# Kernel optimization log

Measured on AMD Instinct MI355X. Metric: run time of the kernel, lower is better.

## Reference

```python
import jax, jax.numpy as jnp
import numpy as np

K = 64            # number of keypoints
PATCH = 16        # patch size
NUM_CLASSES = 1000
K_HARRIS = 0.04


def _conv3x3(x, w):
    # x: [N, Cin, H, W], w: [Cout, Cin, 3, 3], stride 1, padding 1 (torch conv2d = cross-correlation)
    return jax.lax.conv_general_dilated(x, w, (1, 1), 'SAME',
                                        dimension_numbers=('NCHW', 'OIHW', 'NCHW'))


def _harris_coords(x, k, patch_size):
    B, C, H, W = x.shape
    g = jnp.mean(x, axis=1, keepdims=True) if C != 1 else x  # grayscale [B,1,H,W]
    dxk = jnp.array([[-1., 0., 1.], [-1., 0., 1.], [-1., 0., 1.]], x.dtype).reshape(1, 1, 3, 3)
    dyk = jnp.array([[-1., -1., -1.], [0., 0., 0.], [1., 1., 1.]], x.dtype).reshape(1, 1, 3, 3)
    gauss = (jnp.array([[1., 2., 1.], [2., 4., 2.], [1., 2., 1.]], x.dtype) / 16.0).reshape(1, 1, 3, 3)
    dx = _conv3x3(g, dxk)
    dy = _conv3x3(g, dyk)
    Sxx = _conv3x3(dx * dx, gauss)
    Syy = _conv3x3(dy * dy, gauss)
    Sxy = _conv3x3(dx * dy, gauss)
    R = Sxx * Syy - Sxy ** 2 - K_HARRIS * (Sxx + Syy) ** 2  # [B,1,H,W]
    m = patch_size
    mask = jnp.zeros((H, W), x.dtype).at[m:H - m, m:W - m].set(1.0)
    R_flat = (R[:, 0] * mask).reshape(B, -1)
    _, idx = jax.lax.top_k(R_flat, k)                        # [B,k]
    coords = jnp.stack([idx // W, idx % W], axis=-1).astype(jnp.float32)  # (row, col)
    coords = (coords / jnp.array([H, W], jnp.float32) - 0.5) * 2.0
    return jnp.clip(coords, -1.0, 1.0)                       # [B,k,2]


def _grid_sample_bilinear(img, grid):
    # img: [N,C,H,W]; grid: [N,Hg,Wg,2] with (x, y) in [-1,1]; align_corners=True, zeros padding
    N, C, H, W = img.shape
    Hg, Wg = grid.shape[1], grid.shape[2]
    gx = (grid[..., 0] + 1.0) * 0.5 * (W - 1)
    gy = (grid[..., 1] + 1.0) * 0.5 * (H - 1)
    x0 = jnp.floor(gx); y0 = jnp.floor(gy)
    x1 = x0 + 1.0;      y1 = y0 + 1.0
    wx1 = gx - x0; wx0 = 1.0 - wx1
    wy1 = gy - y0; wy0 = 1.0 - wy1

    img_flat = img.reshape(N, C, H * W)

    def gather(xi, yi):
        valid = ((xi >= 0) & (xi < W) & (yi >= 0) & (yi < H)).astype(img.dtype)
        xc = jnp.clip(xi, 0, W - 1).astype(jnp.int32)
        yc = jnp.clip(yi, 0, H - 1).astype(jnp.int32)
        flat = (yc * W + xc).reshape(N, 1, Hg * Wg)
        vals = jnp.take_along_axis(img_flat, flat, axis=2).reshape(N, C, Hg, Wg)
        return vals * valid[:, None]

    out = (gather(x0, y0) * (wx0 * wy0)[:, None]
           + gather(x1, y0) * (wx1 * wy0)[:, None]
           + gather(x0, y1) * (wx0 * wy1)[:, None]
           + gather(x1, y1) * (wx1 * wy1)[:, None])
    return out


def _extract_patches(images, keypoints, patch_size):
    B, C, H, W = images.shape
    k = keypoints.shape[1]
    coords01 = (keypoints + 1.0) / 2.0                       # [B,k,2] (y,x) in [0,1]
    r = patch_size / H
    pg = jnp.linspace(-r, r, patch_size)
    yy, xx = jnp.meshgrid(pg, pg, indexing='ij')
    base = jnp.stack([xx, yy], axis=-1)[None, None]          # [1,1,P,P,2] (x_off, y_off)
    grid = base + coords01[:, :, None, None, :]              # faithful to original broadcast
    grid = grid * 2.0 - 1.0
    grid = grid.reshape(B * k, patch_size, patch_size, 2)
    x_exp = jnp.repeat(images, k, axis=0)                    # repeat_interleave on batch
    patches = _grid_sample_bilinear(x_exp, grid)             # [B*k,C,P,P]
    return patches.reshape(B, k, C, patch_size, patch_size)


def _classify(patches, conv_w, conv_b, fc1_w, fc1_b, fc2_w, fc2_b):
    B, k, C, H, W = patches.shape
    p = patches.reshape(B * k, C, H, W)
    h = _conv3x3(p, conv_w) + conv_b[None, :, None, None]
    h = jax.nn.relu(h)
    h = h.reshape(B * k, -1)                                 # [B*k, 8*P*P]
    h = jax.nn.relu(h @ fc1_w.T + fc1_b)                     # [B*k, 64]
    h = h.reshape(B, k * 64)
    return h @ fc2_w.T + fc2_b                               # [B, num_classes]


def setup_inputs() -> dict:
    key = jax.random.key(0)
    ks = jax.random.split(key, 7)
    B, C, H, W = 32, 3, 224, 224
    return {
        'x': jax.random.normal(ks[0], (B, C, H, W), dtype=jnp.float32),
        'conv_w': jax.random.normal(ks[1], (8, C, 3, 3), dtype=jnp.float32) * 0.1,
        'conv_b': jax.random.normal(ks[2], (8,), dtype=jnp.float32) * 0.05,
        'fc1_w': jax.random.normal(ks[3], (64, 8 * PATCH * PATCH), dtype=jnp.float32) * 0.02,
        'fc1_b': jax.random.normal(ks[4], (64,), dtype=jnp.float32) * 0.05,
        'fc2_w': jax.random.normal(ks[5], (NUM_CLASSES, 64 * K), dtype=jnp.float32) * 0.02,
        'fc2_b': jax.random.normal(ks[6], (NUM_CLASSES,), dtype=jnp.float32) * 0.05,
    }


def reference(x, conv_w, conv_b, fc1_w, fc1_b, fc2_w, fc2_b):
    coords = _harris_coords(x, K, PATCH)                     # [B,K,2]
    patches = _extract_patches(x, coords, PATCH)             # [B,K,C,P,P]
    return _classify(patches, conv_w, conv_b, fc1_w, fc1_b, fc2_w, fc2_b)
```

## Files before the change

kernel.cpp:

```cpp
#include <hip/hip_runtime.h>
#include <cstdint>
#include <math.h>

#define HW 224
#define NPIX (HW*HW)
#define BATCH 32
#define KP 64
#define PS 16
#define NCLS 1000
#define TKB 56
#define FC1_KS 16

__device__ __forceinline__ uint64_t tk_pack(float v, int idx) {
    uint32_t u = __float_as_uint(v);
    u = (u & 0x80000000u) ? ~u : (u | 0x80000000u);
    return ((uint64_t)u << 32) | (uint32_t)(~idx);
}

template<int S>
__device__ __forceinline__ uint64_t sx64(uint64_t k) {
    uint32_t lo = (uint32_t)k, hi = (uint32_t)(k >> 32);
    if constexpr (S == 1) {
        lo = (uint32_t)__builtin_amdgcn_mov_dpp((int)lo, 0xB1, 0xF, 0xF, true);
        hi = (uint32_t)__builtin_amdgcn_mov_dpp((int)hi, 0xB1, 0xF, 0xF, true);
    } else if constexpr (S == 2) {
        lo = (uint32_t)__builtin_amdgcn_mov_dpp((int)lo, 0x4E, 0xF, 0xF, true);
        hi = (uint32_t)__builtin_amdgcn_mov_dpp((int)hi, 0x4E, 0xF, 0xF, true);
    } else if constexpr (S <= 16) {
        constexpr int imm = (S << 10) | 0x1F;
        lo = (uint32_t)__builtin_amdgcn_ds_swizzle((int)lo, imm);
        hi = (uint32_t)__builtin_amdgcn_ds_swizzle((int)hi, imm);
    } else {
        lo = (uint32_t)__shfl_xor((int)lo, 32, 64);
        hi = (uint32_t)__shfl_xor((int)hi, 32, 64);
    }
    return ((uint64_t)hi << 32) | lo;
}

#define BSTAGE(SIZE, S) { uint64_t o = sx64<S>(k); \
    bool keepmax = (((lane & S) != 0) == ((lane & SIZE) == 0)); \
    k = keepmax ? (k > o ? k : o) : (k < o ? k : o); }

__device__ __forceinline__ uint64_t tk_sort_asc(uint64_t k, int lane) {
    BSTAGE(2,1)
    BSTAGE(4,2)  BSTAGE(4,1)
    BSTAGE(8,4)  BSTAGE(8,2)  BSTAGE(8,1)
    BSTAGE(16,8) BSTAGE(16,4) BSTAGE(16,2) BSTAGE(16,1)
    BSTAGE(32,16) BSTAGE(32,8) BSTAGE(32,4) BSTAGE(32,2) BSTAGE(32,1)
    BSTAGE(64,32) BSTAGE(64,16) BSTAGE(64,8) BSTAGE(64,4) BSTAGE(64,2) BSTAGE(64,1)
    return k;
}

#define CSTAGE(S) { uint64_t o = sx64<S>(k); \
    bool keepmax = ((lane & S) == 0); \
    k = keepmax ? (k > o ? k : o) : (k < o ? k : o); }

__device__ __forceinline__ uint64_t tk_clean_desc(uint64_t k, int lane) {
    CSTAGE(32) CSTAGE(16) CSTAGE(8) CSTAGE(4) CSTAGE(2) CSTAGE(1)
    return k;
}

__global__ __launch_bounds__(256) void k_harris_topk(const float* __restrict__ x,
                                                     uint64_t* __restrict__ cand) {
    const int r = blockIdx.x, b = blockIdx.y;
    const int tid = threadIdx.x;
    const int row0 = r * 4;
    __shared__ float G[8][228];
    __shared__ float DXs[6][228];
    __shared__ float DYs[6][228];
    __shared__ float RB[896];
    __shared__ uint64_t SM[4][64];
    const float* xb = x + (size_t)b * 3 * NPIX;

    for (int l = tid; l < 8 * 224; l += 256) {
        int gr = l / 224, gc = l % 224;
        int gy = row0 - 2 + gr;
        float v = 0.f;
        if (gy >= 0 && gy < HW) {
            int o = gy * HW + gc;
            v = (xb[o] + xb[NPIX + o] + xb[2 * NPIX + o]) / 3.0f;
        }
        G[gr][gc + 1] = v;
    }
    if (tid < 8) { G[tid][0] = 0.f; G[tid][225] = 0.f; }
    if (tid < 6) { DXs[tid][0] = 0.f; DXs[tid][225] = 0.f;
                   DYs[tid][0] = 0.f; DYs[tid][225] = 0.f; }
    __syncthreads();

    if (tid < 192) {
        int dr = tid >> 5, cb = (tid & 31) * 7;
        int ay = row0 - 1 + dr;
        float g0[9], g1[9], g2[9];
        #pragma unroll
        for (int v = 0; v < 9; v++) {
            g0[v] = G[dr][cb + v];
            g1[v] = G[dr + 1][cb + v];
            g2[v] = G[dr + 2][cb + v];
        }
        bool ok = (ay >= 0 && ay < HW);
        #pragma unroll
        for (int t = 0; t < 7; t++) {
            float dxv = 0.f, dyv = 0.f;
            if (ok) {
                dxv = (g0[t + 2] - g0[t]) + (g1[t + 2] - g1[t]) +
                      (g2[t + 2] - g2[t]);
                dyv = (g2[t] + g2[t + 1] + g2[t + 2]) -
                      (g0[t] + g0[t + 1] + g0[t + 2]);
            }
            DXs[dr][cb + t + 1] = dxv;
            DYs[dr][cb + t + 1] = dyv;
        }
    }
    __syncthreads();

    if (tid < 128) {
        const int rr = tid >> 5, cb = (tid & 31) * 7;
        const int gy = row0 + rr;
        float dxw[3][9], dyw[3][9];
        #pragma unroll
        for (int u = 0; u < 3; u++)
            #pragma unroll
            for (int v = 0; v < 9; v++) {
                dxw[u][v] = DXs[rr + u][cb + v];
                dyw[u][v] = DYs[rr + u][cb + v];
            }
        const bool rowok = (gy >= PS && gy < HW - PS);
        const float gw[3][3] = {{1.f/16.f, 2.f/16.f, 1.f/16.f},
                                {2.f/16.f, 4.f/16.f, 2.f/16.f},
                                {1.f/16.f, 2.f/16.f, 1.f/16.f}};
        #pragma unroll
        for (int t = 0; t < 7; t++) {
            int c = cb + t;
            float outv = 0.f;
            if (rowok && c >= PS && c < HW - PS) {
                float sxx = 0.f, syy = 0.f, sxy = 0.f;
                #pragma unroll
                for (int u = 0; u < 3; u++)
                    #pragma unroll
                    for (int v = 0; v < 3; v++) {
                        float dv = dxw[u][t + v];
                        float ev = dyw[u][t + v];
                        float w = gw[u][v];
                        sxx += w * dv * dv;
                        syy += w * ev * ev;
                        sxy += w * dv * ev;
                    }
                float tr = sxx + syy;
                outv = sxx * syy - sxy * sxy - 0.04f * tr * tr;
            }
            RB[rr * 224 + c] = outv;
        }
    }
    __syncthreads();

    const int w = tid >> 6, lane = tid & 63;
    const int gbase = (row0 + w) * 224;
    uint64_t T = 0;
    #pragma unroll 1
    for (int it = 0; it < 4; it++) {
        int px = it * 64 + lane;
        uint64_t ck = 0;
        if (px < 224) ck = tk_pack(RB[w * 224 + px], gbase + px);
        uint64_t thr = __shfl(T, 63, 64);
        if (__ballot(ck > thr)) {
            uint64_t s = tk_sort_asc(ck, lane);
            uint64_t m = (T > s) ? T : s;
            T = tk_clean_desc(m, lane);
        }
    }

    SM[w][lane] = T;
    __syncthreads();
    if (w == 0 || w == 2) {
        uint64_t C = SM[w + 1][63 - lane];
        uint64_t m = (T > C) ? T : C;
        T = tk_clean_desc(m, lane);
        SM[w][lane] = T;
    }
    __syncthreads();
    if (w == 0) {
        uint64_t C = SM[2][63 - lane];
        uint64_t m = (T > C) ? T : C;
        T = tk_clean_desc(m, lane);
        cand[((size_t)b * TKB + r) * 64 + lane] = T;
    }
}

__global__ __launch_bounds__(512) void k_topk_merge(const uint64_t* __restrict__ cand,
                                                    int* __restrict__ kp) {
    const int img = blockIdx.x;
    const int w = threadIdx.x >> 6, lane = threadIdx.x & 63;
    const uint64_t* cb = cand + (size_t)img * TKB * 64;
    __shared__ uint64_t S[8][64];

    uint64_t T = cb[(w * 7) * 64 + lane];
    #pragma unroll
    for (int r = 1; r < 7; r++) {
        uint64_t C = cb[(w * 7 + r) * 64 + (63 - lane)];
        uint64_t m = (T > C) ? T : C;
        T = tk_clean_desc(m, lane);
    }
    S[w][lane] = T;
    __syncthreads();
    if (w == 0) {
        #pragma unroll
        for (int r = 1; r < 8; r++) {
            uint64_t C = S[r][63 - lane];
            uint64_t m = (T > C) ? T : C;
            T = tk_clean_desc(m, lane);
        }
        kp[img * KP + lane] = (int)(~(uint32_t)T);
    }
}

__device__ __forceinline__ float gat4(const float* img, float xf, float yf) {
    bool valid = (xf >= 0.f) && (xf < 224.f) && (yf >= 0.f) && (yf < 224.f);
    if (!valid) return 0.f;
    int xi = (int)fminf(fmaxf(xf, 0.f), 223.f);
    int yi = (int)fminf(fmaxf(yf, 0.f), 223.f);
    return img[yi * HW + xi];
}

__global__ __launch_bounds__(256) void k_patch_conv(
    const float* __restrict__ x, const int* __restrict__ kp,
    const float* __restrict__ conv_w, const float* __restrict__ conv_b,
    float* __restrict__ h) {
    const int s = blockIdx.x;
    const int b = blockIdx.y;
    const int tid = threadIdx.x;

    __shared__ float P[3][18][18];

    const int idx = kp[b * KP + s];
    const int row = idx / HW, col = idx % HW;
    float cy = ((float)row / 224.0f - 0.5f) * 2.0f;
    float cx = ((float)col / 224.0f - 0.5f) * 2.0f;
    cy = fminf(fmaxf(cy, -1.0f), 1.0f);
    cx = fminf(fmaxf(cx, -1.0f), 1.0f);
    const float y01 = (cy + 1.0f) * 0.5f;
    const float x01 = (cx + 1.0f) * 0.5f;
    const float rr = 16.0f / 224.0f;
    const float step = (2.0f * rr) / 15.0f;
    const float* xb = x + (size_t)b * 3 * NPIX;

    for (int e = tid; e < 972; e += 256) {
        int c = e / 324, rem = e - c * 324;
        int yy = rem / 18, xx = rem - yy * 18;
        float val = 0.f;
        if (yy >= 1 && yy <= 16 && xx >= 1 && xx <= 16) {
            int i = yy - 1, j = xx - 1;
            float pj = (j == 15) ? rr : (-rr + (float)j * step);
            float pi = (i == 15) ? rr : (-rr + (float)i * step);
            float gxn = (pj + y01) * 2.0f - 1.0f;
            float gyn = (pi + x01) * 2.0f - 1.0f;
            float gx = (gxn + 1.0f) * 0.5f * 223.0f;
            float gy = (gyn + 1.0f) * 0.5f * 223.0f;
            float x0 = floorf(gx), y0 = floorf(gy);
            float x1 = x0 + 1.0f, y1 = y0 + 1.0f;
            float wx1 = gx - x0, wy1 = gy - y0;
            float wx0 = 1.0f - wx1, wy0 = 1.0f - wy1;
            const float* img = xb + (size_t)c * NPIX;
            val = gat4(img, x0, y0) * (wx0 * wy0)
                + gat4(img, x1, y0) * (wx1 * wy0)
                + gat4(img, x0, y1) * (wx0 * wy1)
                + gat4(img, x1, y1) * (wx1 * wy1);
        }
        P[c][yy][xx] = val;
    }
    __syncthreads();

    const int i = tid >> 4, j = tid & 15;
    float acc[8];
    #pragma unroll
    for (int co = 0; co < 8; co++) acc[co] = conv_b[co];
    #pragma unroll
    for (int ci = 0; ci < 3; ci++) {
        float n[9];
        #pragma unroll
        for (int di = 0; di < 3; di++)
            #pragma unroll
            for (int dj = 0; dj < 3; dj++)
                n[di * 3 + dj] = P[ci][i + di][j + dj];
        #pragma unroll
        for (int co = 0; co < 8; co++) {
            float a = acc[co];
            #pragma unroll
            for (int u = 0; u < 9; u++)
                a += n[u] * conv_w[co * 27 + ci * 9 + u];
            acc[co] = a;
        }
    }
    const size_t mbase = ((size_t)(b * KP + s)) * 2048;
    #pragma unroll
    for (int co = 0; co < 8; co++)
        h[mbase + co * 256 + tid] = fmaxf(acc[co], 0.0f);
}

__global__ __launch_bounds__(256) void k_fc1(
    const float* __restrict__ h, const float* __restrict__ fc1_w,
    float* __restrict__ partial) {
    const int mt = blockIdx.x;
    const int ks = blockIdx.y;
    const int tid = threadIdx.x;
    const int M0 = mt * 64;
    const int og = tid >> 4, mg = tid & 15;
    __shared__ float A[64 * 68];
    __shared__ float W[64 * 68];
    float acc[4][4];
    #pragma unroll
    for (int i = 0; i < 4; i++)
        #pragma unroll
        for (int j = 0; j < 4; j++) acc[i][j] = 0.f;

    #pragma unroll 1
    for (int ch = 0; ch < 2; ch++) {
        const int k0 = ks * 128 + ch * 64;
        __syncthreads();
        #pragma unroll
        for (int p = 0; p < 4; p++) {
            int row = p * 16 + (tid >> 4);
            int c0 = (tid & 15) * 4;
            float4 av = *(const float4*)&h[(size_t)(M0 + row) * 2048 + k0 + c0];
            A[(c0 + 0) * 68 + row] = av.x;
            A[(c0 + 1) * 68 + row] = av.y;
            A[(c0 + 2) * 68 + row] = av.z;
            A[(c0 + 3) * 68 + row] = av.w;
            float4 wv = *(const float4*)&fc1_w[(size_t)row * 2048 + k0 + c0];
            W[(c0 + 0) * 68 + row] = wv.x;
            W[(c0 + 1) * 68 + row] = wv.y;
            W[(c0 + 2) * 68 + row] = wv.z;
            W[(c0 + 3) * 68 + row] = wv.w;
        }
        __syncthreads();
        #pragma unroll 4
        for (int k = 0; k < 64; k++) {
            float4 a = *(float4*)&A[k * 68 + mg * 4];
            float4 w = *(float4*)&W[k * 68 + og * 4];
            acc[0][0] += a.x * w.x; acc[0][1] += a.x * w.y;
            acc[0][2] += a.x * w.z; acc[0][3] += a.x * w.w;
            acc[1][0] += a.y * w.x; acc[1][1] += a.y * w.y;
            acc[1][2] += a.y * w.z; acc[1][3] += a.y * w.w;
            acc[2][0] += a.z * w.x; acc[2][1] += a.z * w.y;
            acc[2][2] += a.z * w.z; acc[2][3] += a.z * w.w;
            acc[3][0] += a.w * w.x; acc[3][1] += a.w * w.y;
            acc[3][2] += a.w * w.z; acc[3][3] += a.w * w.w;
        }
    }
    float* pb = partial + ((size_t)ks * 2048 + M0) * 64;
    #pragma unroll
    for (int mi = 0; mi < 4; mi++) {
        float4 v = make_float4(acc[mi][0], acc[mi][1], acc[mi][2], acc[mi][3]);
        *(float4*)&pb[(mg * 4 + mi) * 64 + og * 4] = v;
    }
}

__global__ __launch_bounds__(256) void k_fc1_post(
    const float* __restrict__ partial, const float* __restrict__ fc1_b,
    const float* __restrict__ fc2_b, float* __restrict__ feat,
    float* __restrict__ out) {
    const int id = blockIdx.x * 256 + threadIdx.x;
    const int o = id & 63;
    float s = 0.f;
    #pragma unroll
    for (int ks = 0; ks < FC1_KS; ks++) s += partial[(size_t)ks * 131072 + id];
    s = fmaxf(s + fc1_b[o], 0.f);
    feat[id] = s;
    if (id < BATCH * NCLS) out[id] = fc2_b[id % NCLS];
}

__global__ __launch_bounds__(256) void k_fc2(
    const float* __restrict__ feat, const float* __restrict__ fc2_w,
    float* __restrict__ out) {
    const int c0 = blockIdx.x * 8;
    const int kbase = blockIdx.y * 256;
    const int tid = threadIdx.x;
    const int bq = tid & 7, kg = tid >> 3;

    __shared__ float U[8192];
    float* F2 = U;
    float* Wc = U + 32 * 132;
    float* Red = U;

    float4 acc[8];
    #pragma unroll
    for (int cl = 0; cl < 8; cl++) acc[cl] = make_float4(0.f, 0.f, 0.f, 0.f);

    #pragma unroll 1
    for (int ch = 0; ch < 2; ch++) {
        const int k0 = kbase + ch * 128;
        __syncthreads();
        #pragma unroll
        for (int it = 0; it < 4; it++) {
            int l = it * 256 + tid;
            int bb = l >> 5, kc = (l & 31) << 2;
            *(float4*)&F2[bb * 132 + kc] =
                *(const float4*)&feat[(size_t)bb * 4096 + k0 + kc];
        }
        {
            int cl = tid >> 5, kc = (tid & 31) << 2;
            *(float4*)&Wc[cl * 128 + kc] =
                *(const float4*)&fc2_w[(size_t)(c0 + cl) * 4096 + k0 + kc];
        }
        __syncthreads();
        float4 f0 = *(float4*)&F2[(bq * 4 + 0) * 132 + kg * 4];
        float4 f1 = *(float4*)&F2[(bq * 4 + 1) * 132 + kg * 4];
        float4 f2 = *(float4*)&F2[(bq * 4 + 2) * 132 + kg * 4];
        float4 f3 = *(float4*)&F2[(bq * 4 + 3) * 132 + kg * 4];
        #pragma unroll
        for (int cl = 0; cl < 8; cl++) {
            float4 w = *(float4*)&Wc[cl * 128 + kg * 4];
            acc[cl].x += w.x * f0.x + w.y * f0.y + w.z * f0.z + w.w * f0.w;
            acc[cl].y += w.x * f1.x + w.y * f1.y + w.z * f1.z + w.w * f1.w;
            acc[cl].z += w.x * f2.x + w.y * f2.y + w.z * f2.z + w.w * f2.w;
            acc[cl].w += w.x * f3.x + w.y * f3.y + w.z * f3.z + w.w * f3.w;
        }
    }

    __syncthreads();
    #pragma unroll
    for (int cl = 0; cl < 8; cl++)
        *(float4*)&Red[kg * 256 + cl * 32 + bq * 4] = acc[cl];
    __syncthreads();

    const int cl2 = tid >> 5, b2 = tid & 31;
    float s = 0.f;
    #pragma unroll
    for (int g = 0; g < 32; g++) s += Red[g * 256 + cl2 * 32 + b2];
    atomicAdd(&out[b2 * NCLS + c0 + cl2], s);
}

extern "C" void kernel_launch(void* const* d_in, const int* in_sizes, int n_in,
                              void* d_out, int out_size, void* d_ws, size_t ws_size,
                              hipStream_t stream) {
    const float* x      = (const float*)d_in[0];
    const float* conv_w = (const float*)d_in[1];
    const float* conv_b = (const float*)d_in[2];
    const float* fc1_w  = (const float*)d_in[3];
    const float* fc1_b  = (const float*)d_in[4];
    const float* fc2_w  = (const float*)d_in[5];
    const float* fc2_b  = (const float*)d_in[6];
    float* out = (float*)d_out;

    char* base = (char*)d_ws;
    const size_t region0 = (size_t)FC1_KS * 2048 * 64 * 4;
    uint64_t* cand    = (uint64_t*)base;
    float*    partial = (float*)base;
    float*    h       = (float*)(base + region0);
    float*    feat    = h + (size_t)2048 * 2048;
    int*      kp      = (int*)(feat + (size_t)4096 * 32);

    k_harris_topk<<<dim3(56, 32), 256, 0, stream>>>(x, cand);
    k_topk_merge<<<32, 512, 0, stream>>>(cand, kp);
    k_patch_conv<<<dim3(KP, BATCH), 256, 0, stream>>>(x, kp, conv_w, conv_b, h);
    k_fc1<<<dim3(32, FC1_KS), 256, 0, stream>>>(h, fc1_w, partial);
    k_fc1_post<<<512, 256, 0, stream>>>(partial, fc1_b, fc2_b, feat, out);
    k_fc2<<<dim3(125, 16), 256, 0, stream>>>(feat, fc2_w, out);
}
```

Baseline: 163.5 us.

## Retile Harris kernel into 8-row by 112-column blocks

```diff
diff --git a/kernel.cpp b/kernel.cpp
--- a/kernel.cpp
+++ b/kernel.cpp
@@ -62,67 +62,70 @@
 
 __global__ __launch_bounds__(256) void k_harris_topk(const float* __restrict__ x,
                                                      uint64_t* __restrict__ cand) {
-    const int r = blockIdx.x, b = blockIdx.y;
+    const int r = blockIdx.x;
+    const int hf = blockIdx.y;
+    const int b = blockIdx.z;
     const int tid = threadIdx.x;
-    const int row0 = r * 4;
-    __shared__ float G[8][228];
-    __shared__ float DXs[6][228];
-    __shared__ float DYs[6][228];
-    __shared__ float RB[896];
+    const int row0 = r * 8;
+    const int c0 = hf * 112;
+    __shared__ float U[12 * 120];
+    float (*G)[120] = (float(*)[120])U;
+    float* RB = U;
+    __shared__ float DXs[10][120];
+    __shared__ float DYs[10][120];
     __shared__ uint64_t SM[4][64];
     const float* xb = x + (size_t)b * 3 * NPIX;
 
-    for (int l = tid; l < 8 * 224; l += 256) {
-        int gr = l / 224, gc = l % 224;
+    for (int l = tid; l < 12 * 116; l += 256) {
+        int gr = l / 116, gc = l % 116;
         int gy = row0 - 2 + gr;
+        int gxc = c0 - 2 + gc;
         float v = 0.f;
-        if (gy >= 0 && gy < HW) {
-            int o = gy * HW + gc;
+        if (gy >= 0 && gy < HW && gxc >= 0 && gxc < HW) {
+            int o = gy * HW + gxc;
             v = (xb[o] + xb[NPIX + o] + xb[2 * NPIX + o]) / 3.0f;
         }
-        G[gr][gc + 1] = v;
-    }
-    if (tid < 8) { G[tid][0] = 0.f; G[tid][225] = 0.f; }
-    if (tid < 6) { DXs[tid][0] = 0.f; DXs[tid][225] = 0.f;
-                   DYs[tid][0] = 0.f; DYs[tid][225] = 0.f; }
-    __syncthreads();
-
-    if (tid < 192) {
-        int dr = tid >> 5, cb = (tid & 31) * 7;
+        G[gr][gc] = v;
+    }
+    __syncthreads();
+
+    if (tid < 190) {
+        int dr = tid / 19, rb = (tid % 19) * 6;
         int ay = row0 - 1 + dr;
-        float g0[9], g1[9], g2[9];
-        #pragma unroll
-        for (int v = 0; v < 9; v++) {
-            g0[v] = G[dr][cb + v];
-            g1[v] = G[dr + 1][cb + v];
-            g2[v] = G[dr + 2][cb + v];
-        }
-        bool ok = (ay >= 0 && ay < HW);
-        #pragma unroll
-        for (int t = 0; t < 7; t++) {
+        float g0[8], g1[8], g2[8];
+        #pragma unroll
+        for (int v = 0; v < 8; v++) {
+            g0[v] = G[dr][rb + v];
+            g1[v] = G[dr + 1][rb + v];
+            g2[v] = G[dr + 2][rb + v];
+        }
+        bool okr = (ay >= 0 && ay < HW);
+        #pragma unroll
+        for (int t = 0; t < 6; t++) {
+            int ax = c0 - 1 + rb + t;
             float dxv = 0.f, dyv = 0.f;
-            if (ok) {
+            if (okr && ax >= 0 && ax < HW) {
                 dxv = (g0[t + 2] - g0[t]) + (g1[t + 2] - g1[t]) +
                       (g2[t + 2] - g2[t]);
                 dyv = (g2[t] + g2[t + 1] + g2[t + 2]) -
                       (g0[t] + g0[t + 1] + g0[t + 2]);
             }
-            DXs[dr][cb + t + 1] = dxv;
-            DYs[dr][cb + t + 1] = dyv;
+            DXs[dr][rb + t] = dxv;
+            DYs[dr][rb + t] = dyv;
         }
     }
     __syncthreads();
 
     if (tid < 128) {
-        const int rr = tid >> 5, cb = (tid & 31) * 7;
+        const int rr = tid >> 4, rb = (tid & 15) * 7;
         const int gy = row0 + rr;
         float dxw[3][9], dyw[3][9];
         #pragma unroll
         for (int u = 0; u < 3; u++)
             #pragma unroll
             for (int v = 0; v < 9; v++) {
-                dxw[u][v] = DXs[rr + u][cb + v];
-                dyw[u][v] = DYs[rr + u][cb + v];
+                dxw[u][v] = DXs[rr + u][rb + v];
+                dyw[u][v] = DYs[rr + u][rb + v];
             }
         const bool rowok = (gy >= PS && gy < HW - PS);
         const float gw[3][3] = {{1.f/16.f, 2.f/16.f, 1.f/16.f},
@@ -130,7 +133,7 @@
                                 {1.f/16.f, 2.f/16.f, 1.f/16.f}};
         #pragma unroll
         for (int t = 0; t < 7; t++) {
-            int c = cb + t;
+            int c = c0 + rb + t;
             float outv = 0.f;
             if (rowok && c >= PS && c < HW - PS) {
                 float sxx = 0.f, syy = 0.f, sxy = 0.f;
@@ -148,19 +151,23 @@
                 float tr = sxx + syy;
                 outv = sxx * syy - sxy * sxy - 0.04f * tr * tr;
             }
-            RB[rr * 224 + c] = outv;
+            RB[rr * 112 + rb + t] = outv;
         }
     }
     __syncthreads();
 
     const int w = tid >> 6, lane = tid & 63;
-    const int gbase = (row0 + w) * 224;
     uint64_t T = 0;
     #pragma unroll 1
     for (int it = 0; it < 4; it++) {
         int px = it * 64 + lane;
         uint64_t ck = 0;
-        if (px < 224) ck = tk_pack(RB[w * 224 + px], gbase + px);
+        if (px < 224) {
+            int rl = (px >= 112) ? 1 : 0;
+            int cl = px - rl * 112;
+            ck = tk_pack(RB[w * 224 + px],
+                         (row0 + 2 * w + rl) * 224 + c0 + cl);
+        }
         uint64_t thr = __shfl(T, 63, 64);
         if (__ballot(ck > thr)) {
             uint64_t s = tk_sort_asc(ck, lane);
@@ -182,7 +189,7 @@
         uint64_t C = SM[2][63 - lane];
         uint64_t m = (T > C) ? T : C;
         T = tk_clean_desc(m, lane);
-        cand[((size_t)b * TKB + r) * 64 + lane] = T;
+        cand[((size_t)b * TKB + r * 2 + hf) * 64 + lane] = T;
     }
 }
 
@@ -449,7 +456,7 @@
     float*    feat    = h + (size_t)2048 * 2048;
     int*      kp      = (int*)(feat + (size_t)4096 * 32);
 
-    k_harris_topk<<<dim3(56, 32), 256, 0, stream>>>(x, cand);
+    k_harris_topk<<<dim3(28, 2, 32), 256, 0, stream>>>(x, cand);
     k_topk_merge<<<32, 512, 0, stream>>>(cand, kp);
     k_patch_conv<<<dim3(KP, BATCH), 256, 0, stream>>>(x, kp, conv_w, conv_b, h);
     k_fc1<<<dim3(32, FC1_KS), 256, 0, stream>>>(h, fc1_w, partial);
```

After: 164.9 us. About the same (+0.9%).
